# Kernel optimization log

Measured on AMD Instinct MI355X. Metric: run time of the kernel, lower is better.

Reference implementation:

```python
import jax, jax.numpy as jnp
import numpy as np

S, B, D = 2048, 16, 512  # seq_len, batch, dim_in (= value_dim = key_dim)


def setup_inputs() -> dict:
    key = jax.random.key(0)
    ks = jax.random.split(key, 7)
    scale = 1.0 / np.sqrt(D)
    return {
        "seq": jax.random.normal(ks[0], (S, B, D), dtype=jnp.float32),
        "Wv": jax.random.normal(ks[1], (D, D), dtype=jnp.float32) * scale,
        "bv": jax.random.normal(ks[2], (D,), dtype=jnp.float32) * 0.01,
        "Wq": jax.random.normal(ks[3], (D, D), dtype=jnp.float32) * scale,
        "bq": jax.random.normal(ks[4], (D,), dtype=jnp.float32) * 0.01,
        "Wk": jax.random.normal(ks[5], (D, D), dtype=jnp.float32) * scale,
        "bk": jax.random.normal(ks[6], (D,), dtype=jnp.float32) * 0.01,
    }


def reference(seq, Wv, bv, Wq, bq, Wk, bk):
    # seq: [S, B, D] -> [B, S, D]
    x = jnp.transpose(seq, (1, 0, 2))
    value = x @ Wv.T + bv   # [B, S, Dv]
    query = x @ Wq.T + bq   # [B, S, Dv]
    keys = x @ Wk.T + bk    # [B, S, Dk]
    inv_sqrt_d = 1.0 / np.sqrt(seq.shape[-1]).astype(np.float32)
    # note: scores use value @ query^T (roles swapped vs standard SDPA), per source
    weights = jnp.einsum('bsd,btd->bst', value, query) * inv_sqrt_d  # [B, S, S]
    weights = jax.nn.softmax(weights, axis=-1)
    out = jnp.einsum('bst,btk->bsk', weights, keys)  # [B, S, Dk]
    return jnp.transpose(out, (1, 0, 2))  # [S, B, Dk]
```

## Files before the change

### kernel.cpp

```cpp
#include <hip/hip_runtime.h>
#include <hip/hip_bf16.h>

#define SS 2048
#define BB 16
#define DD 512

typedef __attribute__((ext_vector_type(4))) float f32x4;
typedef __attribute__((ext_vector_type(8))) short bf16x8;
typedef __attribute__((ext_vector_type(4))) unsigned short us4;
typedef unsigned short us;

#define MFMA16(a,b,c) __builtin_amdgcn_mfma_f32_16x16x32_bf16((a),(b),(c),0,0,0)
#define BAR() __builtin_amdgcn_s_barrier()
#define WAITV(n) asm volatile("s_waitcnt vmcnt(" #n ")" ::: "memory")
#define WAITL()  asm volatile("s_waitcnt lgkmcnt(0)" ::: "memory")
#define ADV4(s) s = ((s) + 1) & 3

__device__ __forceinline__ unsigned short f2b(float f) {
    union { float f; unsigned u; } v; v.f = f;
    unsigned r = v.u + 0x7FFFu + ((v.u >> 16) & 1u);
    return (unsigned short)(r >> 16);
}

__device__ __forceinline__ bf16x8 ldfrag8(const us* base, int row, int kelem) {
    int off = (row << 8) + (kelem << 1);
    off ^= (row & 15) << 4;
    return *(const bf16x8*)((const char*)base + off);
}
__device__ __forceinline__ bf16x8 ldfrag(const us* base, int row, int kelem, int rowshift) {
    int off = (row << rowshift) + (kelem << 1);
    off ^= (row & 7) << 4;
    return *(const bf16x8*)((const char*)base + off);
}

__device__ __forceinline__ void gl16(const void* g, void* l) {
    __builtin_amdgcn_global_load_lds(
        (const __attribute__((address_space(1))) unsigned*)g,
        (__attribute__((address_space(3))) unsigned*)l, 16, 0, 0);
}

__global__ __launch_bounds__(256) void k_prep_x(const float* __restrict__ seq,
        us* __restrict__ Xb, us* __restrict__ Xbt) {
    __shared__ __align__(16) char L[64 * 128];
    const int tid = threadIdx.x;
    const int d0 = blockIdx.x * 64, s0 = blockIdx.y * 64, b = blockIdx.z;
    {
        int r = tid >> 2, seg = (tid & 3) * 16;
        const float* src = seq + (size_t)(s0 + r) * (BB * DD) + (size_t)b * DD + d0 + seg;
        __align__(16) us vals[16];
        #pragma unroll
        for (int q = 0; q < 4; ++q) {
            f32x4 v = *(const f32x4*)(src + q * 4);
            vals[q*4+0] = f2b(v.x); vals[q*4+1] = f2b(v.y);
            vals[q*4+2] = f2b(v.z); vals[q*4+3] = f2b(v.w);
        }
        us* xo = Xb + ((size_t)b * SS + s0 + r) * DD + d0 + seg;
        *(bf16x8*)xo       = *(bf16x8*)&vals[0];
        *(bf16x8*)(xo + 8) = *(bf16x8*)&vals[8];
        #pragma unroll
        for (int j = 0; j < 16; ++j) {
            int d = seg + j;
            int addr = (d * 128 + r * 2) ^ ((d & 7) << 4);
            *(us*)(L + addr) = vals[j];
        }
    }
    __syncthreads();
    {
        int d = tid >> 2, sseg = (tid & 3) * 16;
        int c = (d & 7) << 4;
        int base = d * 128 + sseg * 2;
        bf16x8 h0 = *(bf16x8*)(L + (base ^ c));
        bf16x8 h1 = *(bf16x8*)(L + ((base + 16) ^ c));
        us* o = Xbt + ((size_t)b * DD + d0 + d) * SS + s0 + sseg;
        *(bf16x8*)o       = h0;
        *(bf16x8*)(o + 8) = h1;
    }
}

__global__ __launch_bounds__(256) void k_prepG(const float* __restrict__ Wv,
        const float* __restrict__ Wq, us* __restrict__ Gt) {
    __shared__ float Sq[32][64], Sv[32][64];
    const int tid = threadIdx.x;
    const int p0 = blockIdx.x * 64, i0 = blockIdx.y * 64;
    const int tp = tid & 15, ti = tid >> 4;
    float acc[4][4] = {};
    for (int a0 = 0; a0 < DD; a0 += 32) {
        #pragma unroll
        for (int j = 0; j < 2; ++j) {
            int slot = tid + j * 256;
            int row = slot >> 4, c4 = (slot & 15) * 4;
            *(f32x4*)&Sq[row][c4] = *(const f32x4*)(Wq + (size_t)(a0 + row) * DD + p0 + c4);
            *(f32x4*)&Sv[row][c4] = *(const f32x4*)(Wv + (size_t)(a0 + row) * DD + i0 + c4);
        }
        __syncthreads();
        for (int a = 0; a < 32; ++a) {
            f32x4 q = *(f32x4*)&Sq[a][tp * 4];
            f32x4 v = *(f32x4*)&Sv[a][ti * 4];
            #pragma unroll
            for (int x = 0; x < 4; ++x)
                #pragma unroll
                for (int y = 0; y < 4; ++y)
                    acc[x][y] += q[x] * v[y];
        }
        __syncthreads();
    }
    const float sc = 0.044194173824159216f;
    #pragma unroll
    for (int x = 0; x < 4; ++x)
        #pragma unroll
        for (int y = 0; y < 4; ++y)
            Gt[(size_t)(p0 + tp * 4 + x) * DD + i0 + ti * 4 + y] = f2b(acc[x][y] * sc);
}

__global__ __launch_bounds__(512) void k_prepU(const float* __restrict__ Wq,
        const float* __restrict__ bv, float* __restrict__ u) {
    int p = threadIdx.x;
    float s = 0.f;
    for (int a0 = 0; a0 < DD; a0 += 8) {
        #pragma unroll
        for (int j = 0; j < 8; ++j)
            s += bv[a0 + j] * Wq[(size_t)(a0 + j) * DD + p];
    }
    u[p] = s * 0.044194173824159216f;
}

__global__ void k_prepW(const float* __restrict__ Wk, us* __restrict__ Wkb) {
    int i = (blockIdx.x * 256 + threadIdx.x) * 4;
    f32x4 v = *(const f32x4*)(Wk + i);
    us4 o; o.x = f2b(v.x); o.y = f2b(v.y); o.z = f2b(v.z); o.w = f2b(v.w);
    *(us4*)(Wkb + i) = o;
}

template<int OUTMODE>
__global__ __launch_bounds__(256, 2) void k_gemm(
        const us* __restrict__ A, const us* __restrict__ Bm,
        const float* __restrict__ bias, void* __restrict__ outp) {
    __shared__ __align__(16) us As[2][128 * 64];
    __shared__ __align__(16) us Bs[2][128 * 64];
    const int tid = threadIdx.x;
    const int lane = tid & 63;
    const int w = tid >> 6;
    const int wr = w >> 1, wc = w & 1;
    const int l15 = lane & 15, lg = lane >> 4;
    const int b = blockIdx.x >> 4;
    const int s0 = (blockIdx.x & 15) * 128;
    const int n0 = blockIdx.y * 128;
    const char* abase = (const char*)(A + ((size_t)b * SS + s0) * DD);
    const char* bbase = (const char*)Bm + (size_t)n0 * 1024;

    f32x4 acc[4][4];
    #pragma unroll
    for (int m = 0; m < 4; ++m)
        #pragma unroll
        for (int n = 0; n < 4; ++n) acc[m][n] = (f32x4)(0.0f);

    auto stage = [&](int db, int p) {
        #pragma unroll
        for (int j = 0; j < 4; ++j) {
            int x = (tid + j * 256) * 16;
            int gx = x ^ (((x >> 7) & 7) << 4);
            int row = gx >> 7, col = gx & 127;
            gl16(abase + (size_t)row * 1024 + p * 128 + col, (char*)As[db] + x);
            gl16(bbase + (size_t)row * 1024 + p * 128 + col, (char*)Bs[db] + x);
        }
    };

    stage(0, 0);
    for (int p = 0; p < 8; ++p) {
        if (p < 7) { stage((p + 1) & 1, p + 1); WAITV(8); }
        else       { WAITV(0); }
        BAR();
        const us* Ac = As[p & 1]; const us* Bc = Bs[p & 1];
        __builtin_amdgcn_s_setprio(1);
        #pragma unroll
        for (int kk = 0; kk < 2; ++kk) {
            bf16x8 af[4], bfr[4];
            #pragma unroll
            for (int m = 0; m < 4; ++m) af[m]  = ldfrag(Ac, 64 * wr + 16 * m + l15, kk * 32 + 8 * lg, 7);
            #pragma unroll
            for (int n = 0; n < 4; ++n) bfr[n] = ldfrag(Bc, 64 * wc + 16 * n + l15, kk * 32 + 8 * lg, 7);
            #pragma unroll
            for (int m = 0; m < 4; ++m)
                #pragma unroll
                for (int n = 0; n < 4; ++n)
                    acc[m][n] = MFMA16(af[m], bfr[n], acc[m][n]);
        }
        __builtin_amdgcn_s_setprio(0);
        BAR();
    }

    #pragma unroll
    for (int m = 0; m < 4; ++m) {
        #pragma unroll
        for (int n = 0; n < 4; ++n) {
            int col = n0 + 64 * wc + 16 * n + l15;
            float bia = bias[col];
            #pragma unroll
            for (int r = 0; r < 4; ++r) {
                int row = s0 + 64 * wr + 16 * m + 4 * lg + r;
                float v = acc[m][n][r] + bia;
                if (OUTMODE == 0)
                    ((us*)outp)[((size_t)b * SS + row) * DD + col] = f2b(v);
                else
                    ((float*)outp)[((size_t)row * BB + b) * DD + col] = v;
            }
        }
    }
}

__global__ __launch_bounds__(512, 2) void k_attn(
        const us* __restrict__ Vtb, const us* __restrict__ Xb,
        const us* __restrict__ Xbt, us* __restrict__ Ob) {
    __shared__ __align__(16) us BUFS[4][16384];
    __shared__ __align__(16) us Pb[64 * 128];
    __shared__ float red[2][64];

    const int tid = threadIdx.x;
    const int lane = tid & 63;
    const int w = tid >> 6;
    const int rg = w & 3;
    const int cg = w >> 2;
    const int l15 = lane & 15, lg = lane >> 4;

    const int wg = blockIdx.x;
    const int b  = ((wg >> 8) << 3) | (wg & 7);
    const int s0 = ((wg >> 3) & 31) * 64;

    const char* vbase  = (const char*)(Vtb + ((size_t)b * SS + s0) * DD);
    const char* xabase = (const char*)(Xb  + (size_t)b * SS * DD);
    const char* xtbase = (const char*)(Xbt + (size_t)b * DD * SS);

    auto issue = [&](int cflat, us* dst0) {
        int c = cflat & 127;
        int i = c & 7, t0 = (c >> 3) << 7;
        char* dst = (char*)dst0;
        if (i < 4) {
            #pragma unroll
            for (int j = 0; j < 4; ++j) {
                int x = tid * 16 + j * 8192;
                int gx = x ^ (((x >> 8) & 15) << 4);
                int row = gx >> 8, col = gx & 255;
                gl16(xabase + (size_t)(t0 + row) * 1024 + i * 256 + col, dst + x);
            }
        } else {
            #pragma unroll
            for (int j = 0; j < 4; ++j) {
                int x = tid * 16 + j * 8192;
                int gx = x ^ (((x >> 8) & 15) << 4);
                int row = gx >> 8, col = gx & 255;
                gl16(xtbase + (size_t)((i - 4) * 128 + row) * (SS * 2)
                            + (size_t)t0 * 2 + col, dst + x);
            }
        }
    };

    #pragma unroll
    for (int p = 0; p < 4; ++p) {
        #pragma unroll
        for (int j = 0; j < 2; ++j) {
            int x = tid * 16 + j * 8192;
            int gx = x ^ (((x >> 8) & 15) << 4);
            int row = gx >> 8, col = gx & 255;
            gl16(vbase + (size_t)row * 1024 + p * 256 + col,
                 (char*)BUFS[0] + p * 16384 + x);
        }
    }
    WAITV(0); BAR();
    bf16x8 af[16];
    #pragma unroll
    for (int p = 0; p < 4; ++p)
        #pragma unroll
        for (int kk = 0; kk < 4; ++kk)
            af[4 * p + kk] = ldfrag8((const us*)BUFS[0] + p * 8192,
                                     16 * rg + l15, 32 * kk + 8 * lg);
    WAITL(); BAR();

    issue(0, BUFS[0]);
    issue(1, BUFS[1]);
    issue(2, BUFS[2]);
    int wslot = 3, rslot = 0;

    f32x4 accv[4][4];
    #pragma unroll
    for (int ph = 0; ph < 4; ++ph)
        #pragma unroll
        for (int nt = 0; nt < 4; ++nt) accv[ph][nt] = (f32x4)(0.0f);
    float lsum[4] = {0.f, 0.f, 0.f, 0.f};
    const int idx = 16 * rg + 4 * lg;

    for (int step = 0; step < 16; ++step) {
        const int cbase = step * 8;
        f32x4 sacc[4];
        #pragma unroll
        for (int nt = 0; nt < 4; ++nt) sacc[nt] = (f32x4)(0.0f);

        #pragma unroll
        for (int p = 0; p < 4; ++p) {
            issue(cbase + p + 3, BUFS[wslot]); ADV4(wslot);
            WAITV(12); BAR();
            const us* sl = BUFS[rslot]; ADV4(rslot);
            __builtin_amdgcn_s_setprio(1);
            #pragma unroll
            for (int kk = 0; kk < 4; ++kk)
                #pragma unroll
                for (int nt = 0; nt < 4; ++nt) {
                    bf16x8 bq = ldfrag8(sl, 64 * cg + 16 * nt + l15, 32 * kk + 8 * lg);
                    sacc[nt] = MFMA16(af[4 * p + kk], bq, sacc[nt]);
                }
            __builtin_amdgcn_s_setprio(0);
            BAR();
        }

        #pragma unroll
        for (int nt = 0; nt < 4; ++nt)
            #pragma unroll
            for (int ri = 0; ri < 4; ++ri)
                sacc[nt][ri] = __expf(sacc[nt][ri]);
        #pragma unroll
        for (int nt = 0; nt < 4; ++nt)
            #pragma unroll
            for (int ri = 0; ri < 4; ++ri) {
                int row = idx + ri;
                int col = 64 * cg + 16 * nt + l15;
                int off = ((row << 8) + (col << 1)) ^ ((row & 15) << 4);
                *(us*)((char*)Pb + off) = f2b(sacc[nt][ri]);
            }
        #pragma unroll
        for (int ri = 0; ri < 4; ++ri) {
            float s = sacc[0][ri] + sacc[1][ri] + sacc[2][ri] + sacc[3][ri];
            s += __shfl_xor(s, 1); s += __shfl_xor(s, 2);
            s += __shfl_xor(s, 4); s += __shfl_xor(s, 8);
            lsum[ri] += s;
        }
        WAITL(); BAR();
        bf16x8 pa[4];
        #pragma unroll
        for (int kk = 0; kk < 4; ++kk)
            pa[kk] = ldfrag8(Pb, 16 * rg + l15, 32 * kk + 8 * lg);

        #pragma unroll
        for (int p = 0; p < 4; ++p) {
            issue(cbase + p + 7, BUFS[wslot]); ADV4(wslot);
            WAITV(12); BAR();
            const us* sl = BUFS[rslot]; ADV4(rslot);
            __builtin_amdgcn_s_setprio(1);
            #pragma unroll
            for (int kk = 0; kk < 4; ++kk)
                #pragma unroll
                for (int nt = 0; nt < 4; ++nt) {
                    bf16x8 bx = ldfrag8(sl, 64 * cg + 16 * nt + l15, 32 * kk + 8 * lg);
                    accv[p][nt] = MFMA16(pa[kk], bx, accv[p][nt]);
                }
            __builtin_amdgcn_s_setprio(0);
            BAR();
        }
    }

    if (l15 == 0) {
        #pragma unroll
        for (int ri = 0; ri < 4; ++ri)
            red[cg][idx + ri] = lsum[ri];
    }
    WAITL(); BAR();
    float tot[4];
    #pragma unroll
    for (int ri = 0; ri < 4; ++ri)
        tot[ri] = red[0][idx + ri] + red[1][idx + ri];
    us* orow = Ob + ((size_t)b * SS + s0) * DD;
    #pragma unroll
    for (int ph = 0; ph < 4; ++ph)
        #pragma unroll
        for (int nt = 0; nt < 4; ++nt)
            #pragma unroll
            for (int ri = 0; ri < 4; ++ri) {
                int row = idx + ri;
                int e = 128 * ph + 64 * cg + 16 * nt + l15;
                orow[(size_t)row * DD + e] = f2b(accv[ph][nt][ri] / tot[ri]);
            }
}

extern "C" void kernel_launch(void* const* d_in, const int* in_sizes, int n_in,
                              void* d_out, int out_size, void* d_ws, size_t ws_size,
                              hipStream_t stream) {
    const float* seq = (const float*)d_in[0];
    const float* Wv  = (const float*)d_in[1];
    const float* bv  = (const float*)d_in[2];
    const float* Wq  = (const float*)d_in[3];
    const float* Wk  = (const float*)d_in[5];
    const float* bk  = (const float*)d_in[6];

    char* ws = (char*)d_ws;
    us*    Xb  = (us*)ws;
    us*    Xbt = (us*)(ws + (size_t)33554432);
    us*    Vtb = (us*)(ws + (size_t)67108864);
    us*    Gt  = (us*)(ws + (size_t)100663296);
    us*    Wkb = (us*)(ws + (size_t)101187584);
    float* u   = (float*)(ws + (size_t)101711872);

    k_prep_x<<<dim3(8, 32, 16), 256, 0, stream>>>(seq, Xb, Xbt);
    k_prepG<<<dim3(8, 8), 256, 0, stream>>>(Wv, Wq, Gt);
    k_prepU<<<1, 512, 0, stream>>>(Wq, bv, u);
    k_prepW<<<256, 256, 0, stream>>>(Wk, Wkb);

    k_gemm<0><<<dim3(256, 4), 256, 0, stream>>>(Xb, Gt, u, (void*)Vtb);
    k_attn<<<512, 512, 0, stream>>>(Vtb, Xb, Xbt, Vtb);
    k_gemm<1><<<dim3(256, 4), 256, 0, stream>>>(Vtb, Wkb, bk, d_out);
}
```

Before: 357.3 us.

## Software-pipeline QK and PV MFMA phases across steps in flash attention loop

Restructures the main attention loop so each phase interleaves the score MFMAs of the next key block with the PV MFMAs of the current block. Two LDS buffers are loaded per phase instead of one. This cuts the number of barrier-separated phases and gives the compiler more independent MFMA work per barrier, keeping the matrix units busy while softmax waits on LDS. The cost is more complex buffer indexing, wrapped prefetches at the end that are discarded, and higher register pressure from keeping sacc and accv live together.

```diff
diff --git a/kernel.cpp b/kernel.cpp
--- a/kernel.cpp
+++ b/kernel.cpp
@@ -14,7 +14,6 @@
 #define BAR() __builtin_amdgcn_s_barrier()
 #define WAITV(n) asm volatile("s_waitcnt vmcnt(" #n ")" ::: "memory")
 #define WAITL()  asm volatile("s_waitcnt lgkmcnt(0)" ::: "memory")
-#define ADV4(s) s = ((s) + 1) & 3
 
 __device__ __forceinline__ unsigned short f2b(float f) {
     union { float f; unsigned u; } v; v.f = f;
@@ -275,11 +274,6 @@
                                      16 * rg + l15, 32 * kk + 8 * lg);
     WAITL(); BAR();
 
-    issue(0, BUFS[0]);
-    issue(1, BUFS[1]);
-    issue(2, BUFS[2]);
-    int wslot = 3, rslot = 0;
-
     f32x4 accv[4][4];
     #pragma unroll
     for (int ph = 0; ph < 4; ++ph)
@@ -288,29 +282,12 @@
     float lsum[4] = {0.f, 0.f, 0.f, 0.f};
     const int idx = 16 * rg + 4 * lg;
 
-    for (int step = 0; step < 16; ++step) {
-        const int cbase = step * 8;
-        f32x4 sacc[4];
-        #pragma unroll
-        for (int nt = 0; nt < 4; ++nt) sacc[nt] = (f32x4)(0.0f);
-
-        #pragma unroll
-        for (int p = 0; p < 4; ++p) {
-            issue(cbase + p + 3, BUFS[wslot]); ADV4(wslot);
-            WAITV(12); BAR();
-            const us* sl = BUFS[rslot]; ADV4(rslot);
-            __builtin_amdgcn_s_setprio(1);
-            #pragma unroll
-            for (int kk = 0; kk < 4; ++kk)
-                #pragma unroll
-                for (int nt = 0; nt < 4; ++nt) {
-                    bf16x8 bq = ldfrag8(sl, 64 * cg + 16 * nt + l15, 32 * kk + 8 * lg);
-                    sacc[nt] = MFMA16(af[4 * p + kk], bq, sacc[nt]);
-                }
-            __builtin_amdgcn_s_setprio(0);
-            BAR();
-        }
-
+    f32x4 sacc[4];
+    #pragma unroll
+    for (int nt = 0; nt < 4; ++nt) sacc[nt] = (f32x4)(0.0f);
+    bf16x8 pa[4];
+
+    auto softmax = [&]() {
         #pragma unroll
         for (int nt = 0; nt < 4; ++nt)
             #pragma unroll
@@ -333,29 +310,69 @@
             lsum[ri] += s;
         }
         WAITL(); BAR();
-        bf16x8 pa[4];
         #pragma unroll
         for (int kk = 0; kk < 4; ++kk)
             pa[kk] = ldfrag8(Pb, 16 * rg + l15, 32 * kk + 8 * lg);
-
+        #pragma unroll
+        for (int nt = 0; nt < 4; ++nt) sacc[nt] = (f32x4)(0.0f);
+    };
+
+    issue(0, BUFS[0]); issue(1, BUFS[1]); issue(2, BUFS[2]); issue(3, BUFS[3]);
+    #pragma unroll
+    for (int p = 0; p < 4; ++p) {
+        WAITV(12); BAR();
+        const us* sl = BUFS[p];
+        __builtin_amdgcn_s_setprio(1);
+        #pragma unroll
+        for (int kk = 0; kk < 4; ++kk)
+            #pragma unroll
+            for (int nt = 0; nt < 4; ++nt) {
+                bf16x8 bq = ldfrag8(sl, 64 * cg + 16 * nt + l15, 32 * kk + 8 * lg);
+                sacc[nt] = MFMA16(af[4 * p + kk], bq, sacc[nt]);
+            }
+        __builtin_amdgcn_s_setprio(0);
+        BAR();
+        if (p == 0) issue(8 + 0, BUFS[0]);
+        if (p == 1) issue(0 + 4 + 0, BUFS[1]);
+        if (p == 2) issue(8 + 1, BUFS[2]);
+        if (p == 3) issue(0 + 4 + 1, BUFS[3]);
+    }
+    softmax();
+
+    for (int n = 0; n < 16; ++n) {
         #pragma unroll
         for (int p = 0; p < 4; ++p) {
-            issue(cbase + p + 7, BUFS[wslot]); ADV4(wslot);
-            WAITV(12); BAR();
-            const us* sl = BUFS[rslot]; ADV4(rslot);
+            const int m = n * 4 + p;
+            const int sA = (m & 1) * 2, sB = sA + 1;
+            WAITV(8); BAR();
+            const us* slA = BUFS[sA];
+            const us* slB = BUFS[sB];
             __builtin_amdgcn_s_setprio(1);
             #pragma unroll
             for (int kk = 0; kk < 4; ++kk)
                 #pragma unroll
                 for (int nt = 0; nt < 4; ++nt) {
-                    bf16x8 bx = ldfrag8(sl, 64 * cg + 16 * nt + l15, 32 * kk + 8 * lg);
+                    bf16x8 bq = ldfrag8(slA, 64 * cg + 16 * nt + l15, 32 * kk + 8 * lg);
+                    sacc[nt] = MFMA16(af[4 * p + kk], bq, sacc[nt]);
+                }
+            #pragma unroll
+            for (int kk = 0; kk < 4; ++kk)
+                #pragma unroll
+                for (int nt = 0; nt < 4; ++nt) {
+                    bf16x8 bx = ldfrag8(slB, 64 * cg + 16 * nt + l15, 32 * kk + 8 * lg);
                     accv[p][nt] = MFMA16(pa[kk], bx, accv[p][nt]);
                 }
             __builtin_amdgcn_s_setprio(0);
             BAR();
-        }
-    }
-
+            const int q = m + 2;
+            const int np = q >> 2, pp = q & 3;
+            issue(((np + 1) & 15) * 8 + pp, BUFS[sA]);
+            issue((np & 15) * 8 + 4 + pp, BUFS[sB]);
+        }
+        if (n < 15) softmax();
+    }
+
+    WAITV(0);
     if (l15 == 0) {
         #pragma unroll
         for (int ri = 0; ri < 4; ++ri)
```

After: 478.7 us. 1.34x slower.
